# Performance work log

Measured on AMD Instinct MI355X. Metric: run time of the kernel, lower is better.

The kernel has to match this reference:

```python
import jax, jax.numpy as jnp
import numpy as np

LRELU = 0.01
EPS = 1e-5
HEADS = 4


def _ln(x, g, b):
    m = x.mean(-1, keepdims=True)
    v = ((x - m) ** 2).mean(-1, keepdims=True)
    return (x - m) / jnp.sqrt(v + EPS) * g + b


def _mapx(x, w1, b1, g1, be1, w2, b2, g2, be2, w3, b3):
    h = jax.nn.leaky_relu(_ln(x @ w1 + b1, g1, be1), LRELU)
    h = jax.nn.leaky_relu(_ln(h @ w2 + b2, g2, be2), LRELU)
    return h @ w3 + b3


def _mcab(x, y, wq, bq, wk, bk, wv, bv, wo, bo, rescale):
    # spectral (channel-wise) multi-head cross attention: q from x, k/v from y
    b, c, h, w = x.shape
    n = h * w
    xt = x.reshape(b, c, n).transpose(0, 2, 1)  # (b, n, c)
    yt = y.reshape(b, c, n).transpose(0, 2, 1)
    dh = c // HEADS
    q = (xt @ wq + bq).reshape(b, n, HEADS, dh).transpose(0, 2, 3, 1)  # (b,H,dh,n)
    k = (yt @ wk + bk).reshape(b, n, HEADS, dh).transpose(0, 2, 3, 1)
    v = (yt @ wv + bv).reshape(b, n, HEADS, dh).transpose(0, 2, 3, 1)
    q = q / (jnp.linalg.norm(q, axis=-1, keepdims=True) + 1e-8)
    k = k / (jnp.linalg.norm(k, axis=-1, keepdims=True) + 1e-8)
    attn = jax.nn.softmax(jnp.einsum('bhdn,bhen->bhde', q, k) * rescale, axis=-1)  # (b,H,dh,dh)
    out = jnp.einsum('bhde,bhen->bhdn', attn, v)  # (b,H,dh,n)
    out = out.transpose(0, 3, 1, 2).reshape(b, n, c) @ wo + bo
    out = out + xt  # residual
    return out.transpose(0, 2, 1).reshape(b, c, h, w)


def setup_inputs() -> dict:
    key = jax.random.key(0)
    ks = jax.random.split(key, 16)
    B, C, H, W, K = 4, 64, 128, 128, 21
    s = 0.02
    nrm = lambda k, shape: jax.random.normal(k, shape, jnp.float32) * s
    return {
        'x': jax.random.normal(ks[0], (B, C, H, W), jnp.float32),
        'semantic': jax.random.uniform(ks[1], (B, K, H, W), jnp.float32),
        'wa': nrm(ks[2], (1, C, 4)), 'ba': jnp.zeros((1, 4), jnp.float32),
        'wb': nrm(ks[3], (20, C, 3)), 'bb': jnp.zeros((20, 3), jnp.float32),
        'in_w': nrm(ks[4], (C, C)), 'in_b': jnp.zeros((C,), jnp.float32),
        'mx_w1': nrm(ks[5], (C, 2 * C)), 'mx_b1': jnp.zeros((2 * C,), jnp.float32),
        'mx_g1': jnp.ones((2 * C,), jnp.float32), 'mx_be1': jnp.zeros((2 * C,), jnp.float32),
        'mx_w2': nrm(ks[6], (2 * C, 2 * C)), 'mx_b2': jnp.zeros((2 * C,), jnp.float32),
        'mx_g2': jnp.ones((2 * C,), jnp.float32), 'mx_be2': jnp.zeros((2 * C,), jnp.float32),
        'mx_w3': nrm(ks[7], (2 * C, C)), 'mx_b3': jnp.zeros((C,), jnp.float32),
        'wq': nrm(ks[8], (C, C)), 'bq': jnp.zeros((C,), jnp.float32),
        'wk': nrm(ks[9], (C, C)), 'bk': jnp.zeros((C,), jnp.float32),
        'wv': nrm(ks[10], (C, C)), 'bv': jnp.zeros((C,), jnp.float32),
        'wo': nrm(ks[11], (C, C)), 'bo': jnp.zeros((C,), jnp.float32),
        'rescale': jnp.ones((HEADS, 1, 1), jnp.float32),
    }


def reference(x, semantic, wa, ba, wb, bb, in_w, in_b,
              mx_w1, mx_b1, mx_g1, mx_be1, mx_w2, mx_b2, mx_g2, mx_be2,
              mx_w3, mx_b3, wq, bq, wk, bk, wv, bv, wo, bo, rescale):
    sem = jax.nn.relu(semantic)            # (b,K,h,w)
    xh = x.transpose(0, 2, 3, 1)           # (b,h,w,c)
    # per-class mask-multiply: (b,K,h,w,c)
    masked = xh[:, None] * sem[:, :, :, :, None]
    # class 0 gets the extra channel (64 = 1*4 + 20*3)
    feat_a = jnp.einsum('bkhwc,kcd->bkhwd', masked[:, :1], wa) + ba[None, :, None, None, :]
    feat_b = jnp.einsum('bkhwc,kcd->bkhwd', masked[:, 1:], wb) + bb[None, :, None, None, :]
    b, _, h, w, _ = feat_a.shape
    feat_a = feat_a.reshape(b, h, w, 4)
    feat_b = jnp.moveaxis(feat_b, 1, 3).reshape(b, h, w, 60)  # preserve class order
    all_feat = jnp.concatenate([feat_a, feat_b], axis=-1)     # (b,h,w,64)
    y = (all_feat @ in_w + in_b).transpose(0, 3, 1, 2)        # (b,c,h,w)
    xm = _mapx(xh, mx_w1, mx_b1, mx_g1, mx_be1, mx_w2, mx_b2, mx_g2, mx_be2, mx_w3, mx_b3)
    xm = xm.transpose(0, 3, 1, 2)
    return _mcab(xm, y, wq, bq, wk, bk, wv, bv, wo, bo, rescale)
```

## Files before the change

kernel.cpp:

```cpp
#include <hip/hip_runtime.h>
#include <hip/hip_bf16.h>

#define NPX 16384
typedef __attribute__((ext_vector_type(8))) short short8;
typedef __attribute__((ext_vector_type(8))) _Float16 half8;
typedef __attribute__((ext_vector_type(4))) _Float16 half4;
typedef __attribute__((ext_vector_type(4))) float f32x4;

#define DEV static __device__ __forceinline__

#define WAB   0
#define WINW  4096
#define W1T   8192
#define W2T   16384
#define W3T   32768
#define WQT   40960
#define WKV   45056
#define WTOT  53248
#define NZERO 4608

DEV float lrelu(float v) { return v >= 0.f ? v : 0.01f * v; }
DEV short f2h(float f) { _Float16 h = (_Float16)f; return __builtin_bit_cast(short, h); }
DEV float h2f(short s) { return (float)__builtin_bit_cast(_Float16, s); }
DEV f32x4 mfmah(half8 a, half8 b, f32x4 c) {
    return __builtin_amdgcn_mfma_f32_16x16x32_f16(a, b, c, 0, 0, 0);
}

template<int K, int NT, int M>
DEV void gemmM(const short* __restrict__ A, int pitch,
               const short* __restrict__ WB, f32x4 (&acc)[M][NT])
{
    int lane = threadIdx.x & 63;
    int ln = lane & 15, q8 = (lane >> 4) * 8;
    const short* ap = A + (size_t)ln * pitch + q8;
    const short* bp = WB + lane * 8;
#pragma unroll
    for (int c0 = 0; c0 < K; c0 += 32) {
        half8 a[M];
#pragma unroll
        for (int m = 0; m < M; ++m)
            a[m] = *(const half8*)(ap + m * 16 * pitch + c0);
#pragma unroll
        for (int t = 0; t < NT; ++t) {
            half8 b = *(const half8*)(bp + (((c0 >> 5) * NT + t) << 9));
#pragma unroll
            for (int m = 0; m < M; ++m) acc[m][t] = mfmah(a[m], b, acc[m][t]);
        }
    }
}

template<int NT, int M>
DEV void acc_biasM(f32x4 (&acc)[M][NT], const float* __restrict__ bias)
{
    int ln = threadIdx.x & 15;
#pragma unroll
    for (int t = 0; t < NT; ++t) {
        float bv = bias[t * 16 + ln];
        f32x4 v = {bv, bv, bv, bv};
#pragma unroll
        for (int m = 0; m < M; ++m) acc[m][t] = v;
    }
}

template<int NT, int M>
DEV void dstoreM(const f32x4 (&acc)[M][NT], short* sD, int pitch)
{
    int lane = threadIdx.x & 63;
    int ln = lane & 15, r0 = (lane >> 4) * 4;
#pragma unroll
    for (int m = 0; m < M; ++m)
#pragma unroll
        for (int t = 0; t < NT; ++t)
#pragma unroll
            for (int r = 0; r < 4; ++r)
                sD[(m * 16 + r0 + r) * pitch + t * 16 + ln] = f2h(acc[m][t][r]);
}

template<int NT, int M>
DEV void ln_regM(f32x4 (&acc)[M][NT], const float* __restrict__ g, const float* __restrict__ be)
{
    int lane = threadIdx.x & 63, ln = lane & 15;
#pragma unroll
    for (int m = 0; m < M; ++m) {
        f32x4 s = {0,0,0,0}, ss = {0,0,0,0};
#pragma unroll
        for (int t = 0; t < NT; ++t)
#pragma unroll
            for (int r = 0; r < 4; ++r) { float v = acc[m][t][r]; s[r] += v; ss[r] += v * v; }
#pragma unroll
        for (int off = 1; off < 16; off <<= 1)
#pragma unroll
            for (int r = 0; r < 4; ++r) {
                s[r] += __shfl_xor(s[r], off);
                ss[r] += __shfl_xor(ss[r], off);
            }
        f32x4 mm, rs;
#pragma unroll
        for (int r = 0; r < 4; ++r) {
            float mean = s[r] * (1.f / 128.f);
            float var = ss[r] * (1.f / 128.f) - mean * mean;
            mm[r] = mean; rs[r] = rsqrtf(var + 1e-5f);
        }
#pragma unroll
        for (int t = 0; t < NT; ++t) {
            float gg = g[t * 16 + ln], bb = be[t * 16 + ln];
#pragma unroll
            for (int r = 0; r < 4; ++r)
                acc[m][t][r] = lrelu((acc[m][t][r] - mm[r]) * rs[r] * gg + bb);
        }
    }
}

__global__ __launch_bounds__(256) void k_prep(const float* __restrict__ wa,
                                              const float* __restrict__ wb,
                                              const float* __restrict__ in_w,
                                              const float* __restrict__ w1,
                                              const float* __restrict__ w2,
                                              const float* __restrict__ w3,
                                              const float* __restrict__ wq,
                                              const float* __restrict__ wk,
                                              const float* __restrict__ wv,
                                              short* __restrict__ wt,
                                              float* __restrict__ gz)
{
    int idx = blockIdx.x * 256 + threadIdx.x;
    if (idx >= WTOT) {
        int z = idx - WTOT;
        if (z < NZERO) gz[z] = 0.f;
        return;
    }
    int base, ETl;
    if      (idx < WINW) { base = WAB;  ETl = 4; }
    else if (idx < W1T)  { base = WINW; ETl = 4; }
    else if (idx < W2T)  { base = W1T;  ETl = 8; }
    else if (idx < W3T)  { base = W2T;  ETl = 8; }
    else if (idx < WQT)  { base = W3T;  ETl = 4; }
    else if (idx < WKV)  { base = WQT;  ETl = 4; }
    else                 { base = WKV;  ETl = 8; }
    int i = idx - base;
    int frag = i >> 9, wi = i & 511;
    int lane = wi >> 3, kk = wi & 7;
    int ln = lane & 15, qd = lane >> 4;
    int cs = frag / ETl, t = frag % ETl;
    int e = t * 16 + ln;
    int k = cs * 32 + qd * 8 + kk;
    float v;
    if (base == WAB) {
        v = (e < 4) ? wa[k * 4 + e] : wb[((e - 4) / 3) * 192 + k * 3 + ((e - 4) % 3)];
    } else if (base == WINW) {
        v = in_w[k * 64 + e];
    } else if (base == W1T) {
        v = w1[k * 128 + e];
    } else if (base == W2T) {
        v = w2[k * 128 + e];
    } else if (base == W3T) {
        v = w3[k * 64 + e];
    } else if (base == WQT) {
        v = wq[k * 64 + e];
    } else {
        v = (e < 64) ? wk[k * 64 + e] : wv[k * 64 + (e - 64)];
    }
    wt[idx] = f2h(v);
}

__global__ __launch_bounds__(256, 4) void k_main(const float* __restrict__ x,
                                                 const float* __restrict__ sem,
                                                 const float* __restrict__ ba,
                                                 const float* __restrict__ bbv,
                                                 const float* __restrict__ in_b,
                                                 const float* __restrict__ b1,
                                                 const float* __restrict__ g1,
                                                 const float* __restrict__ be1,
                                                 const float* __restrict__ b2,
                                                 const float* __restrict__ g2,
                                                 const float* __restrict__ be2,
                                                 const float* __restrict__ b3,
                                                 const float* __restrict__ bq,
                                                 const float* __restrict__ bk,
                                                 const float* __restrict__ bv,
                                                 const short* __restrict__ wt,
                                                 short* __restrict__ vfrag,
                                                 short* __restrict__ xmfrag,
                                                 float* __restrict__ gram,
                                                 float* __restrict__ nsq)
{
    __shared__ short blob[2][8960];
    const int tid = threadIdx.x, w = tid >> 6, lane = tid & 63;
    const int ln = lane & 15, qd = lane >> 4, r0 = qd * 4;
    const int g = w & 1, role = w >> 1;
    const int pw = blockIdx.x * 64 + g * 32;
    const int b = pw >> 14, n0 = pw & (NPX - 1);
    const float* xb = x + (size_t)b * 64 * NPX;
    short* X  = blob[g];
    short* T  = blob[g] + 2304;
    short* H  = blob[g] + 4608;
    short* KT = X;
    float* scr = (float*)T;

    {
        float vb[16];
#pragma unroll
        for (int t = 0; t < 16; ++t)
            vb[t] = xb[(size_t)(qd * 16 + t) * NPX + n0 + role * 16 + ln];
        short8 lo, hi;
#pragma unroll
        for (int t = 0; t < 8; ++t) { lo[t] = f2h(vb[t]); hi[t] = f2h(vb[8 + t]); }
        *reinterpret_cast<short8*>(&X[(role * 16 + ln) * 72 + qd * 16]) = lo;
        *reinterpret_cast<short8*>(&X[(role * 16 + ln) * 72 + qd * 16 + 8]) = hi;
    }
    __syncthreads();

    f32x4 acc8[2][8];
    if (role == 0) {
        acc_biasM<8, 2>(acc8, b1);
        gemmM<64, 8, 2>(X, 72, wt + W1T, acc8);
    } else {
        f32x4 a1f[2][4];
        {
            f32x4 z = {0,0,0,0};
#pragma unroll
            for (int m = 0; m < 2; ++m)
#pragma unroll
                for (int t = 0; t < 4; ++t) a1f[m][t] = z;
        }
        gemmM<64, 4, 2>(X, 72, wt + WAB, a1f);
#pragma unroll
        for (int t = 0; t < 4; ++t) {
            int j = t * 16 + ln;
            int cls = (j < 4) ? 0 : 1 + (j - 4) / 3;
            float bias = (j < 4) ? ba[j] : bbv[j - 4];
#pragma unroll
            for (int m = 0; m < 2; ++m) {
                f32x4 sm4 = *(const f32x4*)(sem + ((size_t)b * 21 + cls) * NPX + n0 + m * 16 + r0);
#pragma unroll
                for (int r = 0; r < 4; ++r)
                    T[(m * 16 + r0 + r) * 72 + j] = f2h(fmaxf(sm4[r], 0.f) * a1f[m][t][r] + bias);
            }
        }
    }
    __syncthreads();

    f32x4 aqreg[2][4];
    if (role == 0) {
        ln_regM<8, 2>(acc8, g1, be1);
        dstoreM<8, 2>(acc8, H, 136);
        acc_biasM<8, 2>(acc8, b2);
        gemmM<128, 8, 2>(H, 136, wt + W2T, acc8);
        ln_regM<8, 2>(acc8, g2, be2);
        dstoreM<8, 2>(acc8, H, 136);
        f32x4 a4[2][4];
        acc_biasM<4, 2>(a4, b3);
        gemmM<128, 4, 2>(H, 136, wt + W3T, a4);
#pragma unroll
        for (int m = 0; m < 2; ++m) {
            short8 lo, hi;
#pragma unroll
            for (int i = 0; i < 8; ++i) {
                lo[i] = f2h(a4[m][i >> 2][i & 3]);
                hi[i] = f2h(a4[m][2 + (i >> 2)][i & 3]);
            }
            size_t xbase = ((size_t)(pw >> 4) + m) * 1024 + lane * 16;
            *reinterpret_cast<short8*>(xmfrag + xbase) = lo;
            *reinterpret_cast<short8*>(xmfrag + xbase + 8) = hi;
        }
        dstoreM<4, 2>(a4, H, 72);
        acc_biasM<4, 2>(aqreg, bq);
        gemmM<64, 4, 2>(H, 72, wt + WQT, aqreg);
    } else {
        f32x4 a4[2][4];
        acc_biasM<4, 2>(a4, in_b);
        gemmM<64, 4, 2>(T, 72, wt + WINW, a4);
        dstoreM<4, 2>(a4, T, 72);
        f32x4 a3[2][8];
#pragma unroll
        for (int t = 0; t < 8; ++t) {
            float bvv = (t < 4) ? bk[t * 16 + ln] : bv[(t - 4) * 16 + ln];
            f32x4 vv = {bvv, bvv, bvv, bvv};
            a3[0][t] = vv; a3[1][t] = vv;
        }
        gemmM<64, 8, 2>(T, 72, wt + WKV, a3);
#pragma unroll
        for (int t = 0; t < 4; ++t)
#pragma unroll
            for (int m = 0; m < 2; ++m)
#pragma unroll
                for (int r = 0; r < 4; ++r)
                    KT[(t * 16 + ln) * 32 + m * 16 + r0 + r] = f2h(a3[m][t][r]);
#pragma unroll
        for (int t = 4; t < 8; ++t)
#pragma unroll
            for (int m = 0; m < 2; ++m)
#pragma unroll
                for (int r = 0; r < 4; ++r)
                    T[m * 1024 + ((t - 4) >> 1) * 512 +
                      ((((t - 4) & 1) * 2 + (ln >> 3)) & 3) * 128 +
                      (r0 + r) * 8 + (ln & 7)] = f2h(a3[m][t][r]);
#pragma unroll
        for (int it = 0; it < 4; ++it) {
            short8 vv = *(const short8*)(&T[it * 512 + lane * 8]);
            *reinterpret_cast<short8*>(vfrag + ((size_t)(pw >> 4)) * 1024 + it * 512 + lane * 8) = vv;
        }
#pragma unroll
        for (int h = 0; h < 4; ++h) {
            f32x4 akk = {0, 0, 0, 0};
#pragma unroll
            for (int m = 0; m < 2; ++m) {
                half8 ka8 = {0, 0, 0, 0, 0, 0, 0, 0};
#pragma unroll
                for (int r = 0; r < 4; ++r) ka8[r] = (_Float16)a3[m][h][r];
                akk = mfmah(ka8, ka8, akk);
            }
#pragma unroll
            for (int r = 0; r < 4; ++r)
                if (ln == r0 + r) scr[h * 16 + r0 + r] = akk[r];
        }
    }
    __syncthreads();

    if (role == 0) {
#pragma unroll
        for (int h = 0; h < 4; ++h) {
            f32x4 aqk = {0,0,0,0}, aqq = {0,0,0,0};
#pragma unroll
            for (int m = 0; m < 2; ++m) {
                half4 kv4 = *(const half4*)(&KT[(h * 16 + ln) * 32 + m * 16 + r0]);
                half8 qa8 = {0, 0, 0, 0, 0, 0, 0, 0};
                half8 ka8 = {0, 0, 0, 0, 0, 0, 0, 0};
#pragma unroll
                for (int r = 0; r < 4; ++r) {
                    qa8[r] = (_Float16)aqreg[m][h][r];
                    ka8[r] = kv4[r];
                }
                aqk = mfmah(qa8, ka8, aqk);
                aqq = mfmah(qa8, qa8, aqq);
            }
#pragma unroll
            for (int r = 0; r < 4; ++r) {
                int d = r0 + r;
                scr[64 + h * 256 + d * 16 + ln] = aqk[r];
                if (ln == d) scr[1088 + h * 16 + d] = aqq[r];
            }
        }
    }
    __syncthreads();

    const float* s0 = (const float*)(blob[0] + 2304);
    const float* s1 = (const float*)(blob[1] + 2304);
#pragma unroll
    for (int i = 0; i < 4; ++i) {
        int idx = i * 256 + tid;
        atomicAdd(&gram[(size_t)b * 1024 + idx], s0[64 + idx] + s1[64 + idx]);
    }
    if (tid < 64) {
        atomicAdd(&nsq[b * 64 + tid], s0[1088 + tid] + s1[1088 + tid]);
    } else if (tid < 128) {
        int t2 = tid - 64;
        atomicAdd(&nsq[256 + b * 64 + t2], s0[t2] + s1[t2]);
    }
}

__global__ __launch_bounds__(256) void k_out(const float* __restrict__ gram,
                                             const float* __restrict__ nsq,
                                             const float* __restrict__ rescale,
                                             const float* __restrict__ wo,
                                             const short* __restrict__ vfrag,
                                             const short* __restrict__ xmfrag,
                                             const float* __restrict__ bo,
                                             float* __restrict__ out)
{
    __shared__ float s_at[1024];
    __shared__ short mtl[4096];
    int tid = threadIdx.x, w = tid >> 6, lane = tid & 63;
    int ln = lane & 15, qd = lane >> 4;
    int pw = blockIdx.x * 64 + w * 16;
    int b = pw >> 14, n0 = pw & (NPX - 1);
    size_t tile = (size_t)(pw >> 4);

    if (tid < 64) {
        int h = tid >> 4, d = tid & 15;
        float nq = sqrtf(nsq[b * 64 + h * 16 + d]) + 1e-8f;
        float rsc = rescale[h];
        float lg[16];
#pragma unroll
        for (int e = 0; e < 16; ++e) {
            float nk = sqrtf(nsq[256 + b * 64 + h * 16 + e]) + 1e-8f;
            lg[e] = rsc * gram[b * 1024 + h * 256 + d * 16 + e] / (nq * nk);
        }
        float m = lg[0];
#pragma unroll
        for (int e = 1; e < 16; ++e) m = fmaxf(m, lg[e]);
        float ssum = 0.f;
#pragma unroll
        for (int e = 0; e < 16; ++e) { lg[e] = expf(lg[e] - m); ssum += lg[e]; }
        float inv = 1.f / ssum;
#pragma unroll
        for (int e = 0; e < 16; ++e) s_at[h * 256 + d * 16 + e] = lg[e] * inv;
    }
    __syncthreads();

    {
        int he = tid >> 2, h = he >> 4, e = he & 15;
        int cc0 = (tid & 3) * 16;
        int mbase = (he >> 5) * 2048 + ((he >> 3) & 3) * 128 + (he & 7);
#pragma unroll
        for (int cx = 0; cx < 16; ++cx) {
            int cc = cc0 + cx;
            float s = 0.f;
#pragma unroll
            for (int d = 0; d < 16; ++d)
                s = fmaf(s_at[h * 256 + d * 16 + e], wo[(h * 16 + d) * 64 + cc], s);
            mtl[mbase + (cc >> 4) * 512 + (cc & 15) * 8] = f2h(s);
        }
    }
    __syncthreads();

    f32x4 acc[4];
#pragma unroll
    for (int t = 0; t < 4; ++t) {
        float bvv = bo[t * 16 + ln];
        f32x4 v = {bvv, bvv, bvv, bvv};
        acc[t] = v;
    }
    const short* ap = vfrag + tile * 1024 + lane * 8;
#pragma unroll
    for (int cs = 0; cs < 2; ++cs) {
        half8 a = *(const half8*)(ap + cs * 512);
#pragma unroll
        for (int t = 0; t < 4; ++t) {
            half8 bfr = *(const half8*)(&mtl[((cs * 4 + t) << 9) + lane * 8]);
            acc[t] = mfmah(a, bfr, acc[t]);
        }
    }
    short8 x0 = *(const short8*)(xmfrag + tile * 1024 + lane * 16);
    short8 x1 = *(const short8*)(xmfrag + tile * 1024 + lane * 16 + 8);
#pragma unroll
    for (int t = 0; t < 4; ++t) {
        int c = t * 16 + ln;
        f32x4 o;
#pragma unroll
        for (int r = 0; r < 4; ++r) {
            short xv = (t < 2) ? x0[t * 4 + r] : x1[(t - 2) * 4 + r];
            o[r] = acc[t][r] + h2f(xv);
        }
        *reinterpret_cast<f32x4*>(out + ((size_t)b * 64 + c) * NPX + n0 + qd * 4) = o;
    }
}

extern "C" void kernel_launch(void* const* d_in, const int* in_sizes, int n_in,
                              void* d_out, int out_size, void* d_ws, size_t ws_size,
                              hipStream_t stream)
{
    const float* x    = (const float*)d_in[0];
    const float* sem  = (const float*)d_in[1];
    const float* wa   = (const float*)d_in[2];
    const float* ba   = (const float*)d_in[3];
    const float* wb   = (const float*)d_in[4];
    const float* bbv  = (const float*)d_in[5];
    const float* in_w = (const float*)d_in[6];
    const float* in_b = (const float*)d_in[7];
    const float* w1   = (const float*)d_in[8];
    const float* b1   = (const float*)d_in[9];
    const float* g1   = (const float*)d_in[10];
    const float* be1  = (const float*)d_in[11];
    const float* w2   = (const float*)d_in[12];
    const float* b2   = (const float*)d_in[13];
    const float* g2   = (const float*)d_in[14];
    const float* be2  = (const float*)d_in[15];
    const float* w3   = (const float*)d_in[16];
    const float* b3   = (const float*)d_in[17];
    const float* wq   = (const float*)d_in[18];
    const float* bq   = (const float*)d_in[19];
    const float* wk   = (const float*)d_in[20];
    const float* bk   = (const float*)d_in[21];
    const float* wv   = (const float*)d_in[22];
    const float* bv   = (const float*)d_in[23];
    const float* wo   = (const float*)d_in[24];
    const float* bo   = (const float*)d_in[25];
    const float* rescale = (const float*)d_in[26];

    char* wsb = (char*)d_ws;
    short* wt   = (short*)wsb;
    short* vpx  = (short*)(wsb + (1u << 20));
    short* xmp  = (short*)(wsb + (1u << 20) + (8u << 20));
    float* gram = (float*)(wsb + (1u << 20) + (16u << 20));
    float* nsq  = gram + 4096;

    dim3 blk(256);
    k_prep<<<dim3(226), blk, 0, stream>>>(wa, wb, in_w, w1, w2, w3, wq, wk, wv, wt, gram);
    k_main<<<dim3(1024), blk, 0, stream>>>(x, sem, ba, bbv, in_b,
                                           b1, g1, be1, b2, g2, be2, b3, bq, bk, bv,
                                           wt, vpx, xmp, gram, nsq);
    k_out<<<dim3(1024), blk, 0, stream>>>(gram, nsq, rescale, wo, vpx, xmp, bo, (float*)d_out);
}
```

Before: 171.3 us.

## Fuse prep, main and output kernels into one persistent kernel with grid barriers

Merges the weight-prep, main projection and output kernels into a single launch of 1024 blocks that synchronise through atomic-counter grid barriers. The V fragments and xm values stay in shared memory across the barrier instead of being written to and re-read from global workspace. This removes two kernel launches and about 16 MB of global round-trip traffic. In exchange it assumes all 1024 blocks are co-resident (4 per CU via launch bounds), which the spin barrier needs to avoid deadlock, and it adds a memset launch plus barrier spin cost.

```diff
diff --git a/kernel.cpp b/kernel.cpp
--- a/kernel.cpp
+++ b/kernel.cpp
@@ -17,7 +17,7 @@
 #define WQT   40960
 #define WKV   45056
 #define WTOT  53248
-#define NZERO 4608
+#define NBLK  1024u
 
 DEV float lrelu(float v) { return v >= 0.f ? v : 0.01f * v; }
 DEV short f2h(float f) { _Float16 h = (_Float16)f; return __builtin_bit_cast(short, h); }
@@ -26,6 +26,22 @@
     return __builtin_amdgcn_mfma_f32_16x16x32_f16(a, b, c, 0, 0, 0);
 }
 
+DEV void gridbar(unsigned* cnt)
+{
+    __syncthreads();
+    if (threadIdx.x == 0) {
+        __threadfence();
+        atomicAdd(cnt, 1u);
+        int guard = 0;
+        while (atomicAdd(cnt, 0u) < NBLK && guard < (1 << 22)) {
+            ++guard;
+            __builtin_amdgcn_s_sleep(8);
+        }
+        __threadfence();
+    }
+    __syncthreads();
+}
+
 template<int K, int NT, int M>
 DEV void gemmM(const short* __restrict__ A, int pitch,
                const short* __restrict__ WB, f32x4 (&acc)[M][NT])
@@ -111,78 +127,38 @@
     }
 }
 
-__global__ __launch_bounds__(256) void k_prep(const float* __restrict__ wa,
-                                              const float* __restrict__ wb,
-                                              const float* __restrict__ in_w,
-                                              const float* __restrict__ w1,
-                                              const float* __restrict__ w2,
-                                              const float* __restrict__ w3,
-                                              const float* __restrict__ wq,
-                                              const float* __restrict__ wk,
-                                              const float* __restrict__ wv,
-                                              short* __restrict__ wt,
-                                              float* __restrict__ gz)
-{
-    int idx = blockIdx.x * 256 + threadIdx.x;
-    if (idx >= WTOT) {
-        int z = idx - WTOT;
-        if (z < NZERO) gz[z] = 0.f;
-        return;
-    }
-    int base, ETl;
-    if      (idx < WINW) { base = WAB;  ETl = 4; }
-    else if (idx < W1T)  { base = WINW; ETl = 4; }
-    else if (idx < W2T)  { base = W1T;  ETl = 8; }
-    else if (idx < W3T)  { base = W2T;  ETl = 8; }
-    else if (idx < WQT)  { base = W3T;  ETl = 4; }
-    else if (idx < WKV)  { base = WQT;  ETl = 4; }
-    else                 { base = WKV;  ETl = 8; }
-    int i = idx - base;
-    int frag = i >> 9, wi = i & 511;
-    int lane = wi >> 3, kk = wi & 7;
-    int ln = lane & 15, qd = lane >> 4;
-    int cs = frag / ETl, t = frag % ETl;
-    int e = t * 16 + ln;
-    int k = cs * 32 + qd * 8 + kk;
-    float v;
-    if (base == WAB) {
-        v = (e < 4) ? wa[k * 4 + e] : wb[((e - 4) / 3) * 192 + k * 3 + ((e - 4) % 3)];
-    } else if (base == WINW) {
-        v = in_w[k * 64 + e];
-    } else if (base == W1T) {
-        v = w1[k * 128 + e];
-    } else if (base == W2T) {
-        v = w2[k * 128 + e];
-    } else if (base == W3T) {
-        v = w3[k * 64 + e];
-    } else if (base == WQT) {
-        v = wq[k * 64 + e];
-    } else {
-        v = (e < 64) ? wk[k * 64 + e] : wv[k * 64 + (e - 64)];
-    }
-    wt[idx] = f2h(v);
-}
-
-__global__ __launch_bounds__(256, 4) void k_main(const float* __restrict__ x,
-                                                 const float* __restrict__ sem,
-                                                 const float* __restrict__ ba,
-                                                 const float* __restrict__ bbv,
-                                                 const float* __restrict__ in_b,
-                                                 const float* __restrict__ b1,
-                                                 const float* __restrict__ g1,
-                                                 const float* __restrict__ be1,
-                                                 const float* __restrict__ b2,
-                                                 const float* __restrict__ g2,
-                                                 const float* __restrict__ be2,
-                                                 const float* __restrict__ b3,
-                                                 const float* __restrict__ bq,
-                                                 const float* __restrict__ bk,
-                                                 const float* __restrict__ bv,
-                                                 const short* __restrict__ wt,
-                                                 short* __restrict__ vfrag,
-                                                 short* __restrict__ xmfrag,
-                                                 float* __restrict__ gram,
-                                                 float* __restrict__ nsq)
+__global__ __launch_bounds__(256, 4) void k_all(const float* __restrict__ x,
+                                                const float* __restrict__ sem,
+                                                const float* __restrict__ wa,
+                                                const float* __restrict__ ba,
+                                                const float* __restrict__ wb,
+                                                const float* __restrict__ bbv,
+                                                const float* __restrict__ in_w,
+                                                const float* __restrict__ in_b,
+                                                const float* __restrict__ w1,
+                                                const float* __restrict__ b1,
+                                                const float* __restrict__ g1,
+                                                const float* __restrict__ be1,
+                                                const float* __restrict__ w2,
+                                                const float* __restrict__ b2,
+                                                const float* __restrict__ g2,
+                                                const float* __restrict__ be2,
+                                                const float* __restrict__ w3,
+                                                const float* __restrict__ b3,
+                                                const float* __restrict__ wq,
+                                                const float* __restrict__ bq,
+                                                const float* __restrict__ wk,
+                                                const float* __restrict__ bk,
+                                                const float* __restrict__ wv,
+                                                const float* __restrict__ bv,
+                                                const float* __restrict__ wo,
+                                                const float* __restrict__ bo,
+                                                const float* __restrict__ rescale,
+                                                short* __restrict__ wt,
+                                                float* __restrict__ gram,
+                                                float* __restrict__ nsq,
+                                                unsigned* __restrict__ cnt,
+                                                float* __restrict__ out)
 {
     __shared__ short blob[2][8960];
     const int tid = threadIdx.x, w = tid >> 6, lane = tid & 63;
@@ -195,7 +171,47 @@
     short* T  = blob[g] + 2304;
     short* H  = blob[g] + 4608;
     short* KT = X;
-    float* scr = (float*)T;
+    float* scrH = (float*)H;
+    float* scrK = (float*)(X + 2048);
+
+    {
+        int idx = blockIdx.x * 256 + tid;
+        if (idx < WTOT) {
+            int base, ETl;
+            if      (idx < WINW) { base = WAB;  ETl = 4; }
+            else if (idx < W1T)  { base = WINW; ETl = 4; }
+            else if (idx < W2T)  { base = W1T;  ETl = 8; }
+            else if (idx < W3T)  { base = W2T;  ETl = 8; }
+            else if (idx < WQT)  { base = W3T;  ETl = 4; }
+            else if (idx < WKV)  { base = WQT;  ETl = 4; }
+            else                 { base = WKV;  ETl = 8; }
+            int i = idx - base;
+            int frag = i >> 9, wi = i & 511;
+            int lne = wi >> 3, kk = wi & 7;
+            int lnn = lne & 15, qdd = lne >> 4;
+            int cs = frag / ETl, t = frag % ETl;
+            int e = t * 16 + lnn;
+            int k = cs * 32 + qdd * 8 + kk;
+            float v;
+            if (base == WAB) {
+                v = (e < 4) ? wa[k * 4 + e] : wb[((e - 4) / 3) * 192 + k * 3 + ((e - 4) % 3)];
+            } else if (base == WINW) {
+                v = in_w[k * 64 + e];
+            } else if (base == W1T) {
+                v = w1[k * 128 + e];
+            } else if (base == W2T) {
+                v = w2[k * 128 + e];
+            } else if (base == W3T) {
+                v = w3[k * 64 + e];
+            } else if (base == WQT) {
+                v = wq[k * 64 + e];
+            } else {
+                v = (e < 64) ? wk[k * 64 + e] : wv[k * 64 + (e - 64)];
+            }
+            wt[idx] = f2h(v);
+        }
+    }
+    gridbar(cnt);
 
     {
         float vb[16];
@@ -241,6 +257,7 @@
     __syncthreads();
 
     f32x4 aqreg[2][4];
+    f32x4 a4xm[2][4];
     if (role == 0) {
         ln_regM<8, 2>(acc8, g1, be1);
         dstoreM<8, 2>(acc8, H, 136);
@@ -248,22 +265,9 @@
         gemmM<128, 8, 2>(H, 136, wt + W2T, acc8);
         ln_regM<8, 2>(acc8, g2, be2);
         dstoreM<8, 2>(acc8, H, 136);
-        f32x4 a4[2][4];
-        acc_biasM<4, 2>(a4, b3);
-        gemmM<128, 4, 2>(H, 136, wt + W3T, a4);
-#pragma unroll
-        for (int m = 0; m < 2; ++m) {
-            short8 lo, hi;
-#pragma unroll
-            for (int i = 0; i < 8; ++i) {
-                lo[i] = f2h(a4[m][i >> 2][i & 3]);
-                hi[i] = f2h(a4[m][2 + (i >> 2)][i & 3]);
-            }
-            size_t xbase = ((size_t)(pw >> 4) + m) * 1024 + lane * 16;
-            *reinterpret_cast<short8*>(xmfrag + xbase) = lo;
-            *reinterpret_cast<short8*>(xmfrag + xbase + 8) = hi;
-        }
-        dstoreM<4, 2>(a4, H, 72);
+        acc_biasM<4, 2>(a4xm, b3);
+        gemmM<128, 4, 2>(H, 136, wt + W3T, a4xm);
+        dstoreM<4, 2>(a4xm, H, 72);
         acc_biasM<4, 2>(aqreg, bq);
         gemmM<64, 4, 2>(H, 72, wt + WQT, aqreg);
     } else {
@@ -296,11 +300,6 @@
                       ((((t - 4) & 1) * 2 + (ln >> 3)) & 3) * 128 +
                       (r0 + r) * 8 + (ln & 7)] = f2h(a3[m][t][r]);
 #pragma unroll
-        for (int it = 0; it < 4; ++it) {
-            short8 vv = *(const short8*)(&T[it * 512 + lane * 8]);
-            *reinterpret_cast<short8*>(vfrag + ((size_t)(pw >> 4)) * 1024 + it * 512 + lane * 8) = vv;
-        }
-#pragma unroll
         for (int h = 0; h < 4; ++h) {
             f32x4 akk = {0, 0, 0, 0};
 #pragma unroll
@@ -312,7 +311,7 @@
             }
 #pragma unroll
             for (int r = 0; r < 4; ++r)
-                if (ln == r0 + r) scr[h * 16 + r0 + r] = akk[r];
+                if (ln == r0 + r) scrK[h * 16 + r0 + r] = akk[r];
         }
     }
     __syncthreads();
@@ -337,44 +336,36 @@
 #pragma unroll
             for (int r = 0; r < 4; ++r) {
                 int d = r0 + r;
-                scr[64 + h * 256 + d * 16 + ln] = aqk[r];
-                if (ln == d) scr[1088 + h * 16 + d] = aqq[r];
-            }
-        }
-    }
-    __syncthreads();
-
-    const float* s0 = (const float*)(blob[0] + 2304);
-    const float* s1 = (const float*)(blob[1] + 2304);
-#pragma unroll
-    for (int i = 0; i < 4; ++i) {
-        int idx = i * 256 + tid;
-        atomicAdd(&gram[(size_t)b * 1024 + idx], s0[64 + idx] + s1[64 + idx]);
-    }
-    if (tid < 64) {
-        atomicAdd(&nsq[b * 64 + tid], s0[1088 + tid] + s1[1088 + tid]);
-    } else if (tid < 128) {
-        int t2 = tid - 64;
-        atomicAdd(&nsq[256 + b * 64 + t2], s0[t2] + s1[t2]);
-    }
-}
-
-__global__ __launch_bounds__(256) void k_out(const float* __restrict__ gram,
-                                             const float* __restrict__ nsq,
-                                             const float* __restrict__ rescale,
-                                             const float* __restrict__ wo,
-                                             const short* __restrict__ vfrag,
-                                             const short* __restrict__ xmfrag,
-                                             const float* __restrict__ bo,
-                                             float* __restrict__ out)
-{
-    __shared__ float s_at[1024];
-    __shared__ short mtl[4096];
-    int tid = threadIdx.x, w = tid >> 6, lane = tid & 63;
-    int ln = lane & 15, qd = lane >> 4;
-    int pw = blockIdx.x * 64 + w * 16;
-    int b = pw >> 14, n0 = pw & (NPX - 1);
-    size_t tile = (size_t)(pw >> 4);
+                scrH[h * 256 + d * 16 + ln] = aqk[r];
+                if (ln == d) scrH[1024 + h * 16 + d] = aqq[r];
+            }
+        }
+    }
+    __syncthreads();
+
+    {
+        const float* h0 = (const float*)(blob[0] + 4608);
+        const float* h1 = (const float*)(blob[1] + 4608);
+        const float* k0 = (const float*)(blob[0] + 2048);
+        const float* k1 = (const float*)(blob[1] + 2048);
+#pragma unroll
+        for (int i = 0; i < 4; ++i) {
+            int idx = i * 256 + tid;
+            atomicAdd(&gram[(size_t)b * 1024 + idx], h0[idx] + h1[idx]);
+        }
+        if (tid < 64) {
+            atomicAdd(&nsq[b * 64 + tid], h0[1024 + tid] + h1[1024 + tid]);
+        } else if (tid < 128) {
+            int t2 = tid - 64;
+            atomicAdd(&nsq[256 + b * 64 + t2], k0[t2] + k1[t2]);
+        }
+    }
+    __syncthreads();
+    if (role == 0) dstoreM<4, 2>(a4xm, X, 72);
+    gridbar(cnt + 16);
+
+    float* s_at = (float*)(blob[1] + 4608);
+    short* mtl  = blob[0] + 4608;
 
     if (tid < 64) {
         int h = tid >> 4, d = tid & 15;
@@ -414,35 +405,39 @@
     }
     __syncthreads();
 
-    f32x4 acc[4];
-#pragma unroll
-    for (int t = 0; t < 4; ++t) {
-        float bvv = bo[t * 16 + ln];
-        f32x4 v = {bvv, bvv, bvv, bvv};
-        acc[t] = v;
-    }
-    const short* ap = vfrag + tile * 1024 + lane * 8;
-#pragma unroll
-    for (int cs = 0; cs < 2; ++cs) {
-        half8 a = *(const half8*)(ap + cs * 512);
+    {
+        int gC = w >> 1, mC = w & 1;
+        int pwC = blockIdx.x * 64 + w * 16;
+        int n0C = pwC & (NPX - 1);
+        const short* apl = blob[gC] + 2304 + mC * 1024;
+        const short* Xg  = blob[gC];
+        f32x4 acc[4];
 #pragma unroll
         for (int t = 0; t < 4; ++t) {
-            half8 bfr = *(const half8*)(&mtl[((cs * 4 + t) << 9) + lane * 8]);
-            acc[t] = mfmah(a, bfr, acc[t]);
-        }
-    }
-    short8 x0 = *(const short8*)(xmfrag + tile * 1024 + lane * 16);
-    short8 x1 = *(const short8*)(xmfrag + tile * 1024 + lane * 16 + 8);
-#pragma unroll
-    for (int t = 0; t < 4; ++t) {
-        int c = t * 16 + ln;
-        f32x4 o;
-#pragma unroll
-        for (int r = 0; r < 4; ++r) {
-            short xv = (t < 2) ? x0[t * 4 + r] : x1[(t - 2) * 4 + r];
-            o[r] = acc[t][r] + h2f(xv);
-        }
-        *reinterpret_cast<f32x4*>(out + ((size_t)b * 64 + c) * NPX + n0 + qd * 4) = o;
+            float bvv = bo[t * 16 + ln];
+            f32x4 v = {bvv, bvv, bvv, bvv};
+            acc[t] = v;
+        }
+#pragma unroll
+        for (int cs = 0; cs < 2; ++cs) {
+            half8 a = *(const half8*)(apl + cs * 512 + lane * 8);
+#pragma unroll
+            for (int t = 0; t < 4; ++t) {
+                half8 bfr = *(const half8*)(&mtl[((cs * 4 + t) << 9) + lane * 8]);
+                acc[t] = mfmah(a, bfr, acc[t]);
+            }
+        }
+#pragma unroll
+        for (int t = 0; t < 4; ++t) {
+            int c = t * 16 + ln;
+            f32x4 o;
+#pragma unroll
+            for (int r = 0; r < 4; ++r) {
+                short xv = Xg[(mC * 16 + qd * 4 + r) * 72 + c];
+                o[r] = acc[t][r] + h2f(xv);
+            }
+            *reinterpret_cast<f32x4*>(out + ((size_t)b * 64 + c) * NPX + n0C + qd * 4) = o;
+        }
     }
 }
 
@@ -480,15 +475,16 @@
 
     char* wsb = (char*)d_ws;
     short* wt   = (short*)wsb;
-    short* vpx  = (short*)(wsb + (1u << 20));
-    short* xmp  = (short*)(wsb + (1u << 20) + (8u << 20));
-    float* gram = (float*)(wsb + (1u << 20) + (16u << 20));
+    float* gram = (float*)(wsb + (1u << 20));
     float* nsq  = gram + 4096;
-
-    dim3 blk(256);
-    k_prep<<<dim3(226), blk, 0, stream>>>(wa, wb, in_w, w1, w2, w3, wq, wk, wv, wt, gram);
-    k_main<<<dim3(1024), blk, 0, stream>>>(x, sem, ba, bbv, in_b,
-                                           b1, g1, be1, b2, g2, be2, b3, bq, bk, bv,
-                                           wt, vpx, xmp, gram, nsq);
-    k_out<<<dim3(1024), blk, 0, stream>>>(gram, nsq, rescale, wo, vpx, xmp, bo, (float*)d_out);
-}
+    unsigned* cnt = (unsigned*)(nsq + 512);
+    float* outp = (float*)d_out;
+
+    hipMemsetAsync(gram, 0, 4608 * sizeof(float) + 32 * sizeof(unsigned), stream);
+    k_all<<<dim3(NBLK), dim3(256), 0, stream>>>(x, sem, wa, ba, wb, bbv,
+                                                in_w, in_b, w1, b1, g1, be1,
+                                                w2, b2, g2, be2, w3, b3,
+                                                wq, bq, wk, bk, wv, bv,
+                                                wo, bo, rescale,
+                                                wt, gram, nsq, cnt, outp);
+}
```

New measurement: 358.9 us. +109.6%, slower.
